# Kernel tuning notes

Hardware: AMD Instinct MI355X
Metric: run time of the kernel (lower is better)

## Reference

```python
import jax, jax.numpy as jnp
import numpy as np

N_NODES = 50000
N_EDGES = 800000
BATCH = 4
C_IN = 64
C_OUT = 64


def setup_inputs() -> dict:
    key = jax.random.key(0)
    k_x, k_e, k_w1, k_b1, k_w2, k_b2 = jax.random.split(key, 6)
    x = jax.random.normal(k_x, (BATCH, N_NODES, C_IN), dtype=jnp.float32)
    edge_index = jax.random.randint(k_e, (2, N_EDGES), 0, N_NODES, dtype=jnp.int64)
    # Linear weights stored torch-style as (out_features, in_features)
    W1 = jax.random.normal(k_w1, (C_OUT, C_IN), dtype=jnp.float32) * (1.0 / np.sqrt(C_IN))
    b1 = jax.random.normal(k_b1, (C_OUT,), dtype=jnp.float32) * 0.01
    W2 = jax.random.normal(k_w2, (C_OUT, C_OUT), dtype=jnp.float32) * (1.0 / np.sqrt(C_OUT))
    b2 = jax.random.normal(k_b2, (C_OUT,), dtype=jnp.float32) * 0.01
    return {"x": x, "edge_index": edge_index, "W1": W1, "b1": b1, "W2": W2, "b2": b2}


def reference(x, edge_index, W1, b1, W2, b2):
    # GINConv (eps=0, train_eps=False, aggr='add'):
    #   h_i = Linear( x_i + sum_{(j->i) in E} x_j )
    src = edge_index[0]  # message sources (x_j)
    dst = edge_index[1]  # aggregation targets

    def gin_layer(h, W, b):
        # scatter-add over the node axis (PyG node_dim=-2), batch broadcast on axis 0
        agg = jnp.zeros_like(h).at[:, dst, :].add(h[:, src, :])  # (B, N, C)
        return (h + agg) @ W.T + b

    h = gin_layer(x, W1, b1)
    h = gin_layer(h, W2, b2)
    return h
```

## Files before the change

### kernel.cpp

```cpp
#include <hip/hip_runtime.h>

#define C_DIM 64
#define B_DIM 4

typedef unsigned short u16;
typedef unsigned int u32;
typedef __attribute__((ext_vector_type(8))) short s16x8;
typedef __attribute__((ext_vector_type(4))) float f32x4;

__device__ __forceinline__ u16 f2bf(float f) {
    union { u32 u; float f; } t; t.f = f;
    u32 u = t.u;
    return (u16)((u + 0x7FFF + ((u >> 16) & 1)) >> 16);
}
__device__ __forceinline__ float lo16(u32 u) {
    union { u32 v; float f; } t; t.v = u << 16; return t.f;
}
__device__ __forceinline__ float hi16(u32 u) {
    union { u32 v; float f; } t; t.v = u & 0xffff0000u; return t.f;
}
__device__ __forceinline__ int pad8(int v) { return (v + 7) & ~7; }

__global__ __launch_bounds__(256) void k_pre(
    const float* __restrict__ in, u16* __restrict__ outb, u16* __restrict__ outb2,
    int n_nodes, const int* __restrict__ dst, int* __restrict__ counts,
    int n_edges, int cvt_blocks, int hist_blocks)
{
    int bid = (int)blockIdx.x;
    if (bid < cvt_blocks) {
        int i = bid * 256 + threadIdx.x;
        if (i >= n_nodes * 32) return;
        int n = i >> 5;
        int r = i & 31;
        int b = r >> 3, c8 = (r & 7) << 3;
        const float4* p = (const float4*)(in + ((size_t)b * n_nodes + n) * 64 + c8);
        float4 A = p[0], B = p[1];
        ushort4 lo, hi;
        lo.x = f2bf(A.x); lo.y = f2bf(A.y); lo.z = f2bf(A.z); lo.w = f2bf(A.w);
        hi.x = f2bf(B.x); hi.y = f2bf(B.y); hi.z = f2bf(B.z); hi.w = f2bf(B.w);
        ushort4* q = (ushort4*)(outb + (size_t)n * 256 + b * 64 + c8);
        q[0] = lo; q[1] = hi;
    } else if (bid < cvt_blocks + hist_blocks) {
        int e = (bid - cvt_blocks) * 256 + threadIdx.x;
        if (e < n_edges) atomicAdd(&counts[dst[e]], 1);
    } else {
        outb [(size_t)n_nodes * 256 + threadIdx.x] = 0;
        outb2[(size_t)n_nodes * 256 + threadIdx.x] = 0;
    }
}


__global__ __launch_bounds__(256) void k_part(
    const int* __restrict__ counts, int* __restrict__ partials, int n_nodes)
{
    __shared__ int s[256];
    int i = blockIdx.x * 256 + threadIdx.x;
    int v = (i < n_nodes) ? pad8(counts[i]) : 0;
    s[threadIdx.x] = v;
    __syncthreads();
    for (int d = 128; d > 0; d >>= 1) {
        if (threadIdx.x < d) s[threadIdx.x] += s[threadIdx.x + d];
        __syncthreads();
    }
    if (threadIdx.x == 0) partials[blockIdx.x] = s[0];
}

__global__ __launch_bounds__(256) void k_scan1(
    int* __restrict__ partials, int nb)
{
    __shared__ int s[256];
    int tid = threadIdx.x;
    int v = (tid < nb) ? partials[tid] : 0;
    s[tid] = v;
    __syncthreads();
    for (int d = 1; d < 256; d <<= 1) {
        int t = (tid >= d) ? s[tid - d] : 0;
        __syncthreads();
        s[tid] += t;
        __syncthreads();
    }
    if (tid < nb) partials[tid] = s[tid] - v;
}

__global__ __launch_bounds__(256) void k_final(
    const int* __restrict__ counts, const int* __restrict__ partials,
    int* __restrict__ offsets, int* __restrict__ cursor, int n_nodes)
{
    __shared__ int s[256];
    int tid = threadIdx.x;
    int i = blockIdx.x * 256 + tid;
    int v = (i < n_nodes) ? pad8(counts[i]) : 0;
    s[tid] = v;
    __syncthreads();
    for (int d = 1; d < 256; d <<= 1) {
        int t = (tid >= d) ? s[tid - d] : 0;
        __syncthreads();
        s[tid] += t;
        __syncthreads();
    }
    if (i < n_nodes) {
        int off = partials[blockIdx.x] + s[tid] - v;
        offsets[i] = off;
        cursor[i] = off;
        if (i == n_nodes - 1) offsets[n_nodes] = off + v;
    }
}

__global__ __launch_bounds__(256) void k_fillp(
    const int* __restrict__ src, const int* __restrict__ dst,
    int* __restrict__ cursor, u16* __restrict__ elist,
    const int* __restrict__ offsets, const int* __restrict__ counts,
    int n_nodes, int n_edges, int fill_blocks, int sentinel)
{
    if ((int)blockIdx.x < fill_blocks) {
        int e = blockIdx.x * 256 + threadIdx.x;
        if (e < n_edges) {
            int pos = atomicAdd(&cursor[dst[e]], 1);
            elist[pos] = (u16)src[e];
        }
    } else {
        int i = (blockIdx.x - fill_blocks) * 256 + threadIdx.x;
        if (i < n_nodes) {
            int e0 = offsets[i] + counts[i];
            int e1 = offsets[i + 1];
            for (int e = e0; e < e1; ++e) elist[e] = (u16)sentinel;
        }
    }
}

__global__ __launch_bounds__(256, 8) void k_gmm2(
    const u16* __restrict__ hb, const u16* __restrict__ elist,
    const int* __restrict__ offsets,
    const float* __restrict__ W,
    const float* __restrict__ bias,
    float* __restrict__ out_f32,
    u16* __restrict__ out_bf,
    int n_nodes)
{
    __shared__ __align__(16) u32 lds[2][16][36];
    u32* lf = &lds[0][0][0];
    int tid = threadIdx.x;
    int w  = tid >> 6;
    int l  = tid & 63;
    int lr = l & 15, lk = l >> 4;
    int h  = blockIdx.x & 1;

    for (int i = tid; i < 2 * 16 * 36; i += 256) lf[i] = 0u;

    s16x8 bf0, bf1;
    {
        const float* wp = W + (w * 16 + lr) * 64 + lk * 8;
        s16x8 f0, f1;
#pragma unroll
        for (int e = 0; e < 8; ++e) {
            f0[e] = (short)f2bf(wp[e]);
            f1[e] = (short)f2bf(wp[e + 32]);
        }
        bf0 = f0; bf1 = f1;
    }
    float bia = bias[w * 16 + lr];

    const int NT = n_nodes >> 2;
    const u16* px = hb + (h << 7) + (l << 1);
    int wword = (((w << 2) | (h << 1) | (l >> 5)) * 36) + (l & 31);
    int rsel = h << 1;

    __syncthreads();

    int buf = 0;
    int step = gridDim.x >> 1;
    for (int tl = blockIdx.x >> 1; tl < NT; tl += step, buf ^= 1) {
        int node = tl * 4 + w;
        int ks = __builtin_amdgcn_readfirstlane(offsets[node]);
        int ke = __builtin_amdgcn_readfirstlane(offsets[node + 1]);
        u32 sv = *(const u32*)(px + ((size_t)node << 8));
        float a0 = lo16(sv), a1 = hi16(sv);
        int nb = (ke - ks) >> 3;
        uint4 I = make_uint4(0u, 0u, 0u, 0u);
        if (nb > 0) I = *(const uint4*)(elist + ks);
        int k = ks;
        for (int bb = 0; bb < nb; ++bb) {
            uint4 In = I;
            if (bb + 1 < nb) In = *(const uint4*)(elist + k + 8);
            u32 s0 = I.x & 0xffffu, s1 = I.x >> 16;
            u32 s2 = I.y & 0xffffu, s3 = I.y >> 16;
            u32 s4 = I.z & 0xffffu, s5 = I.z >> 16;
            u32 s6 = I.w & 0xffffu, s7 = I.w >> 16;
            u32 v0 = *(const u32*)(px + ((size_t)s0 << 8));
            u32 v1 = *(const u32*)(px + ((size_t)s1 << 8));
            u32 v2 = *(const u32*)(px + ((size_t)s2 << 8));
            u32 v3 = *(const u32*)(px + ((size_t)s3 << 8));
            u32 v4 = *(const u32*)(px + ((size_t)s4 << 8));
            u32 v5 = *(const u32*)(px + ((size_t)s5 << 8));
            u32 v6 = *(const u32*)(px + ((size_t)s6 << 8));
            u32 v7 = *(const u32*)(px + ((size_t)s7 << 8));
            asm volatile("" ::
                "v"(v0), "v"(v1), "v"(v2), "v"(v3),
                "v"(v4), "v"(v5), "v"(v6), "v"(v7));
            a0 += lo16(v0); a1 += hi16(v0);
            a0 += lo16(v1); a1 += hi16(v1);
            a0 += lo16(v2); a1 += hi16(v2);
            a0 += lo16(v3); a1 += hi16(v3);
            a0 += lo16(v4); a1 += hi16(v4);
            a0 += lo16(v5); a1 += hi16(v5);
            a0 += lo16(v6); a1 += hi16(v6);
            a0 += lo16(v7); a1 += hi16(v7);
            I = In; k += 8;
        }
        lf[buf * 576 + wword] = (u32)f2bf(a0) | ((u32)f2bf(a1) << 16);
        __syncthreads();

        const u32* lp = lf + buf * 576 + lr * 36 + (lk << 2);
        s16x8 av0 = *(const s16x8*)(lp);
        s16x8 av1 = *(const s16x8*)(lp + 16);

        f32x4 acc = (f32x4){bia, bia, bia, bia};
        acc = __builtin_amdgcn_mfma_f32_16x16x32_bf16(av0, bf0, acc, 0, 0, 0);
        acc = __builtin_amdgcn_mfma_f32_16x16x32_bf16(av1, bf1, acc, 0, 0, 0);

        int R0 = tl * 16 + (lk << 2) + rsel;
        if (out_bf) {
            out_bf[(size_t)R0 * 64 + w * 16 + lr]       = f2bf(acc[rsel]);
            out_bf[(size_t)(R0 + 1) * 64 + w * 16 + lr] = f2bf(acc[rsel + 1]);
        }
        if (out_f32) {
            int n0 = R0 >> 2, b0 = R0 & 3;
            out_f32[(((size_t)b0 * n_nodes + n0) << 6) + w * 16 + lr] = acc[rsel];
            int R1 = R0 + 1;
            int n1 = R1 >> 2, b1 = R1 & 3;
            out_f32[(((size_t)b1 * n_nodes + n1) << 6) + w * 16 + lr] = acc[rsel + 1];
        }
    }
}


__global__ __launch_bounds__(256) void gin_scatter(
    const float* __restrict__ h, const int* __restrict__ src,
    const int* __restrict__ dst, float* __restrict__ agg,
    int n_edges, int n_nodes)
{
    long long i = (long long)blockIdx.x * blockDim.x + threadIdx.x;
    int e = (int)(i >> 6);
    if (e >= n_edges) return;
    int lane = (int)(i & 63);
    int b  = lane >> 4;
    int c4 = (lane & 15) << 2;
    int s = src[e];
    int d = dst[e];
    const float4 v = *reinterpret_cast<const float4*>(
        h + ((size_t)b * n_nodes + s) * C_DIM + c4);
    float* o = agg + ((size_t)b * n_nodes + d) * C_DIM + c4;
    unsafeAtomicAdd(o + 0, v.x);
    unsafeAtomicAdd(o + 1, v.y);
    unsafeAtomicAdd(o + 2, v.z);
    unsafeAtomicAdd(o + 3, v.w);
}

__global__ __launch_bounds__(256) void gin_mm(
    const float* __restrict__ hin, const float* __restrict__ agg,
    const float* __restrict__ W, const float* __restrict__ bias,
    float* __restrict__ out, int M)
{
    __shared__ float Ws[64][65];
    __shared__ float rows[4][64];
    int tid = threadIdx.x;
    for (int i = tid; i < 64 * 64; i += 256)
        Ws[i >> 6][i & 63] = W[i];
    int rloc = tid >> 6;
    int j    = tid & 63;
    int row  = blockIdx.x * 4 + rloc;
    if (row < M)
        rows[rloc][j] = hin[(size_t)row * C_DIM + j] + agg[(size_t)row * C_DIM + j];
    __syncthreads();
    if (row < M) {
        float acc = bias[j];
#pragma unroll
        for (int k = 0; k < 64; ++k)
            acc += rows[rloc][k] * Ws[j][k];
        out[(size_t)row * C_DIM + j] = acc;
    }
}


static inline size_t align256(size_t x) { return (x + 255) & ~(size_t)255; }

extern "C" void kernel_launch(void* const* d_in, const int* in_sizes, int n_in,
                              void* d_out, int out_size, void* d_ws, size_t ws_size,
                              hipStream_t stream)
{
    const float* x   = (const float*)d_in[0];
    const int*   ei  = (const int*)d_in[1];
    const float* W1  = (const float*)d_in[2];
    const float* b1  = (const float*)d_in[3];
    const float* W2  = (const float*)d_in[4];
    const float* b2  = (const float*)d_in[5];
    float* out = (float*)d_out;

    const int n_nodes = in_sizes[0] / (B_DIM * C_DIM);
    const int n_edges = in_sizes[1] / 2;
    const int M = B_DIM * n_nodes;
    const size_t elems = (size_t)M * C_DIM;

    const int* src = ei;
    const int* dst = ei + n_edges;
    const int NB = (n_nodes + 255) / 256;

    const size_t elist_cap = (size_t)n_edges + 8u * (size_t)n_nodes;

    size_t off = 0;
    size_t o_bufA    = off; off = align256(off + (elems + 256) * sizeof(u16));
    size_t o_bufB    = off; off = align256(off + (elems + 256) * sizeof(u16));
    size_t o_counts  = off; off = align256(off + (size_t)n_nodes * sizeof(int));
    size_t o_offsets = off; off = align256(off + (size_t)(n_nodes + 1) * sizeof(int));
    size_t o_cursor  = off; off = align256(off + (size_t)n_nodes * sizeof(int));
    size_t o_part    = off; off = align256(off + 256 * sizeof(int));
    size_t o_elist   = off; off = align256(off + elist_cap * sizeof(u16));
    const size_t need = off;

    const bool fast = (ws_size >= need) && (n_nodes <= 65535) && (NB <= 256) &&
                      ((elems & 7) == 0) && ((n_nodes & 3) == 0);

    dim3 blk(256);

    if (fast) {
        char* ws = (char*)d_ws;
        u16* bufA    = (u16*)(ws + o_bufA);
        u16* bufB    = (u16*)(ws + o_bufB);
        int* counts  = (int*)(ws + o_counts);
        int* offsets = (int*)(ws + o_offsets);
        int* cursor  = (int*)(ws + o_cursor);
        int* partials= (int*)(ws + o_part);
        u16* elist   = (u16*)(ws + o_elist);

        const int cvt_blocks  = (n_nodes * 32 + 255) / 256;
        const int hist_blocks = (n_edges + 255) / 256;
        const int node_blocks = (n_nodes + 255) / 256;
        dim3 grid_pre((unsigned)(cvt_blocks + hist_blocks + 1));
        dim3 grid_n((unsigned)NB);
        dim3 grid_fp((unsigned)(hist_blocks + node_blocks));
        dim3 grid_g(2048);

        hipMemsetAsync(counts, 0, (size_t)n_nodes * sizeof(int), stream);
        k_pre<<<grid_pre, blk, 0, stream>>>(x, bufA, bufB, n_nodes, dst, counts,
                                            n_edges, cvt_blocks, hist_blocks);
        k_part<<<grid_n, blk, 0, stream>>>(counts, partials, n_nodes);
        k_scan1<<<1, blk, 0, stream>>>(partials, NB);
        k_final<<<grid_n, blk, 0, stream>>>(counts, partials, offsets, cursor, n_nodes);
        k_fillp<<<grid_fp, blk, 0, stream>>>(src, dst, cursor, elist, offsets,
                                             counts, n_nodes, n_edges,
                                             hist_blocks, n_nodes);

        k_gmm2<<<grid_g, blk, 0, stream>>>(bufA, elist, offsets, W1, b1,
                                           nullptr, bufB, n_nodes);
        k_gmm2<<<grid_g, blk, 0, stream>>>(bufB, elist, offsets, W2, b2,
                                           out, nullptr, n_nodes);
    } else {
        float* agg = (float*)d_ws;
        const size_t h_bytes = elems * sizeof(float);
        dim3 grid_sc((unsigned)(((long long)n_edges * 64 + 255) / 256));
        dim3 grid_mm((unsigned)((M + 3) / 4));

        hipMemsetAsync(agg, 0, h_bytes, stream);
        gin_scatter<<<grid_sc, blk, 0, stream>>>(x, src, dst, agg, n_edges, n_nodes);
        gin_mm<<<grid_mm, blk, 0, stream>>>(x, agg, W1, b1, out, M);

        hipMemsetAsync(agg, 0, h_bytes, stream);
        gin_scatter<<<grid_sc, blk, 0, stream>>>(out, src, dst, agg, n_edges, n_nodes);
        gin_mm<<<grid_mm, blk, 0, stream>>>(out, agg, W2, b2, out, M);
    }
}
```

Baseline: 214.5 us.

## Split gather work by edge parity across half-waves and fold scan kernel

The gather-matmul kernel now assigns each block one of four batch slices instead of two. Within a wave, the two half-waves take alternating edges (even or odd) and combine their partial sums with a cross-lane shuffle before the MFMA stage, and the inner loop is unrolled two chunks deep. The single-block partial scan kernel is folded into k_final, which rescans the block partials itself, removing one launch. The cost is redundant scanning in every block and twice as many blocks walking each node's edge list, each doing half the gathers.

```diff
diff --git a/kernel.cpp b/kernel.cpp
--- a/kernel.cpp
+++ b/kernel.cpp
@@ -65,29 +65,24 @@
     if (threadIdx.x == 0) partials[blockIdx.x] = s[0];
 }
 
-__global__ __launch_bounds__(256) void k_scan1(
-    int* __restrict__ partials, int nb)
-{
+__global__ __launch_bounds__(256) void k_final(
+    const int* __restrict__ counts, const int* __restrict__ partials,
+    int* __restrict__ offsets, int* __restrict__ cursor, int n_nodes, int nb)
+{
+    __shared__ int sp[256];
     __shared__ int s[256];
     int tid = threadIdx.x;
-    int v = (tid < nb) ? partials[tid] : 0;
-    s[tid] = v;
+    int pv = (tid < nb) ? partials[tid] : 0;
+    sp[tid] = pv;
     __syncthreads();
     for (int d = 1; d < 256; d <<= 1) {
-        int t = (tid >= d) ? s[tid - d] : 0;
-        __syncthreads();
-        s[tid] += t;
-        __syncthreads();
-    }
-    if (tid < nb) partials[tid] = s[tid] - v;
-}
-
-__global__ __launch_bounds__(256) void k_final(
-    const int* __restrict__ counts, const int* __restrict__ partials,
-    int* __restrict__ offsets, int* __restrict__ cursor, int n_nodes)
-{
-    __shared__ int s[256];
-    int tid = threadIdx.x;
+        int t = (tid >= d) ? sp[tid - d] : 0;
+        __syncthreads();
+        sp[tid] += t;
+        __syncthreads();
+    }
+    int base = (blockIdx.x == 0) ? 0 : sp[blockIdx.x - 1];
+
     int i = blockIdx.x * 256 + tid;
     int v = (i < n_nodes) ? pad8(counts[i]) : 0;
     s[tid] = v;
@@ -99,7 +94,7 @@
         __syncthreads();
     }
     if (i < n_nodes) {
-        int off = partials[blockIdx.x] + s[tid] - v;
+        int off = base + s[tid] - v;
         offsets[i] = off;
         cursor[i] = off;
         if (i == n_nodes - 1) offsets[n_nodes] = off + v;
@@ -128,7 +123,7 @@
     }
 }
 
-__global__ __launch_bounds__(256, 8) void k_gmm2(
+__global__ __launch_bounds__(256, 8) void k_gmmq(
     const u16* __restrict__ hb, const u16* __restrict__ elist,
     const int* __restrict__ offsets,
     const float* __restrict__ W,
@@ -143,7 +138,9 @@
     int w  = tid >> 6;
     int l  = tid & 63;
     int lr = l & 15, lk = l >> 4;
-    int h  = blockIdx.x & 1;
+    int q  = blockIdx.x & 3;
+    int p  = l >> 5;
+    int c  = l & 31;
 
     for (int i = tid; i < 2 * 16 * 36; i += 256) lf[i] = 0u;
 
@@ -161,53 +158,77 @@
     float bia = bias[w * 16 + lr];
 
     const int NT = n_nodes >> 2;
-    const u16* px = hb + (h << 7) + (l << 1);
-    int wword = (((w << 2) | (h << 1) | (l >> 5)) * 36) + (l & 31);
-    int rsel = h << 1;
+    const u16* px = hb + (q << 6) + (c << 1);
+    int lrow = (w * 4 + q) * 36 + c;
 
     __syncthreads();
 
     int buf = 0;
-    int step = gridDim.x >> 1;
-    for (int tl = blockIdx.x >> 1; tl < NT; tl += step, buf ^= 1) {
+    int step = gridDim.x >> 2;
+    for (int tl = blockIdx.x >> 2; tl < NT; tl += step, buf ^= 1) {
         int node = tl * 4 + w;
         int ks = __builtin_amdgcn_readfirstlane(offsets[node]);
         int ke = __builtin_amdgcn_readfirstlane(offsets[node + 1]);
         u32 sv = *(const u32*)(px + ((size_t)node << 8));
-        float a0 = lo16(sv), a1 = hi16(sv);
-        int nb = (ke - ks) >> 3;
+        float a0 = p ? 0.f : lo16(sv);
+        float a1 = p ? 0.f : hi16(sv);
+        int ne8 = (ke - ks) >> 3;
         uint4 I = make_uint4(0u, 0u, 0u, 0u);
-        if (nb > 0) I = *(const uint4*)(elist + ks);
+        if (ne8 > 0) I = *(const uint4*)(elist + ks);
         int k = ks;
-        for (int bb = 0; bb < nb; ++bb) {
+        int b = 0;
+        for (; b + 2 <= ne8; b += 2) {
+            uint4 I2 = *(const uint4*)(elist + k + 8);
+            u32 e0 = p ? (I.x >> 16) : (I.x & 0xffffu);
+            u32 e1 = p ? (I.y >> 16) : (I.y & 0xffffu);
+            u32 e2 = p ? (I.z >> 16) : (I.z & 0xffffu);
+            u32 e3 = p ? (I.w >> 16) : (I.w & 0xffffu);
+            u32 v0 = *(const u32*)(px + ((size_t)e0 << 8));
+            u32 v1 = *(const u32*)(px + ((size_t)e1 << 8));
+            u32 v2 = *(const u32*)(px + ((size_t)e2 << 8));
+            u32 v3 = *(const u32*)(px + ((size_t)e3 << 8));
+            u32 f0 = p ? (I2.x >> 16) : (I2.x & 0xffffu);
+            u32 f1 = p ? (I2.y >> 16) : (I2.y & 0xffffu);
+            u32 f2 = p ? (I2.z >> 16) : (I2.z & 0xffffu);
+            u32 f3 = p ? (I2.w >> 16) : (I2.w & 0xffffu);
+            u32 g0 = *(const u32*)(px + ((size_t)f0 << 8));
+            u32 g1 = *(const u32*)(px + ((size_t)f1 << 8));
+            u32 g2 = *(const u32*)(px + ((size_t)f2 << 8));
+            u32 g3 = *(const u32*)(px + ((size_t)f3 << 8));
             uint4 In = I;
-            if (bb + 1 < nb) In = *(const uint4*)(elist + k + 8);
-            u32 s0 = I.x & 0xffffu, s1 = I.x >> 16;
-            u32 s2 = I.y & 0xffffu, s3 = I.y >> 16;
-            u32 s4 = I.z & 0xffffu, s5 = I.z >> 16;
-            u32 s6 = I.w & 0xffffu, s7 = I.w >> 16;
-            u32 v0 = *(const u32*)(px + ((size_t)s0 << 8));
-            u32 v1 = *(const u32*)(px + ((size_t)s1 << 8));
-            u32 v2 = *(const u32*)(px + ((size_t)s2 << 8));
-            u32 v3 = *(const u32*)(px + ((size_t)s3 << 8));
-            u32 v4 = *(const u32*)(px + ((size_t)s4 << 8));
-            u32 v5 = *(const u32*)(px + ((size_t)s5 << 8));
-            u32 v6 = *(const u32*)(px + ((size_t)s6 << 8));
-            u32 v7 = *(const u32*)(px + ((size_t)s7 << 8));
+            if (b + 2 < ne8) In = *(const uint4*)(elist + k + 16);
             asm volatile("" ::
                 "v"(v0), "v"(v1), "v"(v2), "v"(v3),
-                "v"(v4), "v"(v5), "v"(v6), "v"(v7));
+                "v"(g0), "v"(g1), "v"(g2), "v"(g3));
             a0 += lo16(v0); a1 += hi16(v0);
             a0 += lo16(v1); a1 += hi16(v1);
             a0 += lo16(v2); a1 += hi16(v2);
             a0 += lo16(v3); a1 += hi16(v3);
-            a0 += lo16(v4); a1 += hi16(v4);
-            a0 += lo16(v5); a1 += hi16(v5);
-            a0 += lo16(v6); a1 += hi16(v6);
-            a0 += lo16(v7); a1 += hi16(v7);
-            I = In; k += 8;
-        }
-        lf[buf * 576 + wword] = (u32)f2bf(a0) | ((u32)f2bf(a1) << 16);
+            a0 += lo16(g0); a1 += hi16(g0);
+            a0 += lo16(g1); a1 += hi16(g1);
+            a0 += lo16(g2); a1 += hi16(g2);
+            a0 += lo16(g3); a1 += hi16(g3);
+            I = In; k += 16;
+        }
+        if (b < ne8) {
+            u32 e0 = p ? (I.x >> 16) : (I.x & 0xffffu);
+            u32 e1 = p ? (I.y >> 16) : (I.y & 0xffffu);
+            u32 e2 = p ? (I.z >> 16) : (I.z & 0xffffu);
+            u32 e3 = p ? (I.w >> 16) : (I.w & 0xffffu);
+            u32 v0 = *(const u32*)(px + ((size_t)e0 << 8));
+            u32 v1 = *(const u32*)(px + ((size_t)e1 << 8));
+            u32 v2 = *(const u32*)(px + ((size_t)e2 << 8));
+            u32 v3 = *(const u32*)(px + ((size_t)e3 << 8));
+            asm volatile("" :: "v"(v0), "v"(v1), "v"(v2), "v"(v3));
+            a0 += lo16(v0); a1 += hi16(v0);
+            a0 += lo16(v1); a1 += hi16(v1);
+            a0 += lo16(v2); a1 += hi16(v2);
+            a0 += lo16(v3); a1 += hi16(v3);
+        }
+        a0 += __shfl_xor(a0, 32);
+        a1 += __shfl_xor(a1, 32);
+        if (l < 32)
+            lf[buf * 576 + lrow] = (u32)f2bf(a0) | ((u32)f2bf(a1) << 16);
         __syncthreads();
 
         const u32* lp = lf + buf * 576 + lr * 36 + (lk << 2);
@@ -218,18 +239,13 @@
         acc = __builtin_amdgcn_mfma_f32_16x16x32_bf16(av0, bf0, acc, 0, 0, 0);
         acc = __builtin_amdgcn_mfma_f32_16x16x32_bf16(av1, bf1, acc, 0, 0, 0);
 
-        int R0 = tl * 16 + (lk << 2) + rsel;
-        if (out_bf) {
-            out_bf[(size_t)R0 * 64 + w * 16 + lr]       = f2bf(acc[rsel]);
-            out_bf[(size_t)(R0 + 1) * 64 + w * 16 + lr] = f2bf(acc[rsel + 1]);
-        }
-        if (out_f32) {
-            int n0 = R0 >> 2, b0 = R0 & 3;
-            out_f32[(((size_t)b0 * n_nodes + n0) << 6) + w * 16 + lr] = acc[rsel];
-            int R1 = R0 + 1;
-            int n1 = R1 >> 2, b1 = R1 & 3;
-            out_f32[(((size_t)b1 * n_nodes + n1) << 6) + w * 16 + lr] = acc[rsel + 1];
-        }
+        float o = (q & 2) ? ((q & 1) ? acc[3] : acc[2])
+                          : ((q & 1) ? acc[1] : acc[0]);
+        int R0 = tl * 16 + (lk << 2) + q;
+        if (out_bf)
+            out_bf[(size_t)R0 * 64 + w * 16 + lr] = f2bf(o);
+        if (out_f32)
+            out_f32[(((size_t)q * n_nodes + (R0 >> 2)) << 6) + w * 16 + lr] = o;
     }
 }
 
@@ -344,15 +360,15 @@
         k_pre<<<grid_pre, blk, 0, stream>>>(x, bufA, bufB, n_nodes, dst, counts,
                                             n_edges, cvt_blocks, hist_blocks);
         k_part<<<grid_n, blk, 0, stream>>>(counts, partials, n_nodes);
-        k_scan1<<<1, blk, 0, stream>>>(partials, NB);
-        k_final<<<grid_n, blk, 0, stream>>>(counts, partials, offsets, cursor, n_nodes);
+        k_final<<<grid_n, blk, 0, stream>>>(counts, partials, offsets, cursor,
+                                            n_nodes, NB);
         k_fillp<<<grid_fp, blk, 0, stream>>>(src, dst, cursor, elist, offsets,
                                              counts, n_nodes, n_edges,
                                              hist_blocks, n_nodes);
 
-        k_gmm2<<<grid_g, blk, 0, stream>>>(bufA, elist, offsets, W1, b1,
+        k_gmmq<<<grid_g, blk, 0, stream>>>(bufA, elist, offsets, W1, b1,
                                            nullptr, bufB, n_nodes);
-        k_gmm2<<<grid_g, blk, 0, stream>>>(bufB, elist, offsets, W2, b2,
+        k_gmmq<<<grid_g, blk, 0, stream>>>(bufB, elist, offsets, W2, b2,
                                            out, nullptr, n_nodes);
     } else {
         float* agg = (float*)d_ws;
```

Result: slower. 221.8 us (+3.4%).
